# Kernel optimization log

Measured on AMD Instinct MI355X. Metric: run time of the kernel, lower is better.

The kernel has to match this reference:

```python
import jax, jax.numpy as jnp
import numpy as np

P = 200_000   # pedestrians
T = 16        # frames in targets/outputs
F_DIR = 15    # tracklet_length - 5 frames used by direction loss


def _conv_bbox(b):
    # Faithful to the source's in-place convert_bbox, which (due to sequential
    # in-place updates) maps [a,b,c,d] -> [a-c/2, b-d/2, a, b].
    a, bb, c, d = b[..., 0], b[..., 1], b[..., 2], b[..., 3]
    return jnp.stack([a - 0.5 * c, bb - 0.5 * d, a, bb], axis=-1)


def _corner_pts(b):
    # 5 reference points: center, lt(x0,y0), rt(x0,y1), lb(x1,y0), rb(x1,y1)
    x0, y0, x1, y1 = b[..., 0], b[..., 1], b[..., 2], b[..., 3]
    xs = jnp.stack([0.5 * (x0 + x1), x0, x0, x1, x1], axis=-1)
    ys = jnp.stack([0.5 * (y0 + y1), y0, y1, y0, y1], axis=-1)
    return xs, ys


def _unit_dir(fx, fy, tx, ty):
    dy, dx = ty - fy, tx - fx
    n = jnp.sqrt(dy * dy + dx * dx) + 1e-6
    return dy / n, dx / n


def _direction_loss(outputs, targets):
    last = targets[:F_DIR, :, :4]
    pred = last + outputs[:F_DIR]
    true = targets[1:F_DIR + 1, :, :4]
    # Source mutates `targets` in place: frames 1..14 get convert_bbox applied
    # TWICE when reused as `last_abs` (once as prior frame's true_abs). Replicate.
    last_c1 = _conv_bbox(last)
    last_eff = jnp.concatenate([last_c1[:1], _conv_bbox(last_c1[1:])], axis=0)
    pred_c = _conv_bbox(pred)
    true_c = _conv_bbox(true)
    lx, ly = _corner_pts(last_eff)   # [F_DIR, P, 5]
    px, py = _corner_pts(pred_c)
    tx, ty = _corner_pts(true_c)
    pdy, pdx = _unit_dir(lx, ly, px, py)
    tdy, tdx = _unit_dir(lx, ly, tx, ty)
    cosang = jnp.clip(pdy * tdy + pdx * tdx, -1.0, 1.0)
    weight = 0.2
    return weight * jnp.sum(jnp.arccos(cosang)) / (targets.shape[1] * F_DIR)


def setup_inputs() -> dict:
    key = jax.random.key(0)
    k1, k2 = jax.random.split(key)
    outputs = jax.random.normal(k1, (T, P, 4), dtype=jnp.float32) * 0.1
    targets = jax.random.uniform(k2, (T, P, 8), dtype=jnp.float32)
    return {"outputs": outputs, "targets": targets}


def reference(outputs, targets):
    delta = targets[:, :, 4:8]
    d = outputs - delta
    ad = jnp.abs(d)
    sl1 = jnp.where(ad < 1.0, 0.5 * d * d, ad - 0.5)  # smooth_l1, beta=1
    loss_o = jnp.sum(sl1, axis=2) / targets.shape[1]   # [T, P]
    loss_dir = _direction_loss(outputs, targets)
    return 0.99 * loss_o + 0.01 * loss_dir
```

## Files before the change

kernel.cpp:

```cpp
#include <hip/hip_runtime.h>

#define BS 256
#define LD4(ptr) (*reinterpret_cast<const float4*>(ptr))

__device__ __forceinline__ float fast_acos(float x) {
    float ax = fabsf(x);
    float s  = __builtin_amdgcn_sqrtf(fmaxf(0.f, 1.f - ax));
    float p  = fmaf(ax, fmaf(ax, fmaf(ax, -0.0187293f, 0.0742610f), -0.2121144f), 1.5707288f);
    float r  = s * p;
    return (x >= 0.f) ? r : 3.14159265358979f - r;
}

__device__ __forceinline__ float ang(float p2, float t2, float dot) {
    float inv = __builtin_amdgcn_rsqf(p2 * t2);
    float c   = __builtin_amdgcn_fmed3f(dot * inv, -1.f, 1.f);
    return fast_acos(c);
}

__device__ __forceinline__ float dir_item(float4 L, float4 O, float4 Tn, bool first) {
    float pa = L.x + O.x, pb = L.y + O.y;
    float Px0 = pa - 0.5f * (L.z + O.z), Py0 = pb - 0.5f * (L.w + O.w);
    float Px1 = pa, Py1 = pb;
    float Tx0 = Tn.x - 0.5f * Tn.z, Ty0 = Tn.y - 0.5f * Tn.w;
    float Tx1 = Tn.x, Ty1 = Tn.y;
    float Lx1 = L.x - 0.5f * L.z, Ly1 = L.y - 0.5f * L.w;
    float Lx0, Ly0;
    if (first) { Lx0 = Lx1; Ly0 = Ly1; Lx1 = L.x; Ly1 = L.y; }
    else       { Lx0 = 0.5f * (L.x - L.z); Ly0 = 0.5f * (L.y - L.w); }

    float ax0 = Px0 - Lx0, ax1 = Px1 - Lx1, ay0 = Py0 - Ly0, ay1 = Py1 - Ly1;
    float bx0 = Tx0 - Lx0, bx1 = Tx1 - Lx1, by0 = Ty0 - Ly0, by1 = Ty1 - Ly1;
    float acx = 0.5f * (ax0 + ax1), acy = 0.5f * (ay0 + ay1);
    float bcx = 0.5f * (bx0 + bx1), bcy = 0.5f * (by0 + by1);
    float sax0 = ax0 * ax0, sax1 = ax1 * ax1, say0 = ay0 * ay0, say1 = ay1 * ay1;
    float sbx0 = bx0 * bx0, sbx1 = bx1 * bx1, sby0 = by0 * by0, sby1 = by1 * by1;
    float cx0 = ax0 * bx0, cx1 = ax1 * bx1, cy0 = ay0 * by0, cy1 = ay1 * by1;

    float acc;
    acc  = ang(fmaf(acx, acx, acy * acy), fmaf(bcx, bcx, bcy * bcy),
               fmaf(acx, bcx, acy * bcy));
    acc += ang(sax0 + say0, sbx0 + sby0, cx0 + cy0);
    acc += ang(sax0 + say1, sbx0 + sby1, cx0 + cy1);
    acc += ang(sax1 + say0, sbx1 + sby0, cx1 + cy0);
    acc += ang(sax1 + say1, sbx1 + sby1, cx1 + cy1);
    return acc;
}

__device__ __forceinline__ float sl1_4(float4 O, float4 D) {
    float s = 0.f;
    { float d = O.x - D.x, ad = fabsf(d); s += (ad < 1.f) ? 0.5f * d * d : ad - 0.5f; }
    { float d = O.y - D.y, ad = fabsf(d); s += (ad < 1.f) ? 0.5f * d * d : ad - 0.5f; }
    { float d = O.z - D.z, ad = fabsf(d); s += (ad < 1.f) ? 0.5f * d * d : ad - 0.5f; }
    { float d = O.w - D.w, ad = fabsf(d); s += (ad < 1.f) ? 0.5f * d * d : ad - 0.5f; }
    return s;
}

__global__ __launch_bounds__(BS)
void fused_kernel(const float* __restrict__ outputs,
                  const float* __restrict__ targets,
                  float* __restrict__ out,
                  float* __restrict__ partials,
                  int P, float w) {
    __shared__ float smem[BS / 64];
    long long gid = (long long)blockIdx.x * BS + threadIdx.x;
    float acc = 0.f;
    if (gid < 4ll * P) {
        int grp     = (int)(gid / P);
        long long p = gid - (long long)grp * P;
        const long long ts8 = 8ll * P, os4 = 4ll * P;
        const float* tb = targets + ((long long)(grp * 4) * P + p) * 8;
        const float* ob = outputs + ((long long)(grp * 4) * P + p) * 4;
        float*       wb = out + (long long)(grp * 4) * P + p;
        const bool has4 = (grp < 3);

        float4 Tf0 = LD4(tb);
        float4 Tf1 = LD4(tb + ts8);
        float4 Tf2 = LD4(tb + 2 * ts8);
        float4 Tf3 = LD4(tb + 3 * ts8);
        float4 Ts0 = LD4(tb + 4);
        float4 Ts1 = LD4(tb + ts8 + 4);
        float4 Ts2 = LD4(tb + 2 * ts8 + 4);
        float4 Ts3 = LD4(tb + 3 * ts8 + 4);
        float4 O0  = LD4(ob);
        float4 O1  = LD4(ob + os4);
        float4 O2  = LD4(ob + 2 * os4);
        float4 O3  = LD4(ob + 3 * os4);
        float4 Tf4 = has4 ? LD4(tb + 4 * ts8) : make_float4(0.f, 0.f, 0.f, 0.f);

        wb[0]       = sl1_4(O0, Ts0) * w;
        wb[P]       = sl1_4(O1, Ts1) * w;
        wb[2ll * P] = sl1_4(O2, Ts2) * w;
        wb[3ll * P] = sl1_4(O3, Ts3) * w;

        acc  = dir_item(Tf0, O0, Tf1, grp == 0);
        acc += dir_item(Tf1, O1, Tf2, false);
        acc += dir_item(Tf2, O2, Tf3, false);
        if (has4) acc += dir_item(Tf3, O3, Tf4, false);
    }
    #pragma unroll
    for (int off = 32; off > 0; off >>= 1) acc += __shfl_down(acc, off, 64);
    int lane = threadIdx.x & 63, w64 = threadIdx.x >> 6;
    if (lane == 0) smem[w64] = acc;
    __syncthreads();
    if (threadIdx.x == 0) {
        float r = 0.f;
        #pragma unroll
        for (int i = 0; i < BS / 64; ++i) r += smem[i];
        partials[blockIdx.x] = r;
    }
}

__global__ void finalize_kernel(const float* __restrict__ partials, int nb,
                                float* __restrict__ out, long long n4, int P) {
    __shared__ double dsm[BS / 64];
    __shared__ float c_sh;
    double dacc = 0.0;
    for (int i = threadIdx.x; i < nb; i += BS) dacc += (double)partials[i];
    #pragma unroll
    for (int off = 32; off > 0; off >>= 1) dacc += __shfl_down(dacc, off, 64);
    int lane = threadIdx.x & 63, w = threadIdx.x >> 6;
    if (lane == 0) dsm[w] = dacc;
    __syncthreads();
    if (threadIdx.x == 0) {
        double tot = dsm[0] + dsm[1] + dsm[2] + dsm[3];
        c_sh = (float)(0.01 * 0.2 * tot / ((double)P * 15.0));
    }
    __syncthreads();
    float c = c_sh;

    float4* o4 = reinterpret_cast<float4*>(out);
    long long stride = (long long)gridDim.x * blockDim.x;
    for (long long i = (long long)blockIdx.x * blockDim.x + threadIdx.x; i < n4; i += stride) {
        float4 v = o4[i];
        v.x += c; v.y += c; v.z += c; v.w += c;
        o4[i] = v;
    }
}

extern "C" void kernel_launch(void* const* d_in, const int* in_sizes, int n_in,
                              void* d_out, int out_size, void* d_ws, size_t ws_size,
                              hipStream_t stream) {
    const float* outputs = (const float*)d_in[0];
    const float* targets = (const float*)d_in[1];
    float* out = (float*)d_out;
    float* partials = (float*)d_ws;

    const int T = 16;
    int P = in_sizes[0] / (T * 4);

    long long units = 4ll * P;
    int nb1 = (int)((units + BS - 1) / BS);

    fused_kernel<<<nb1, BS, 0, stream>>>(outputs, targets, out, partials,
                                         P, 0.99f / (float)P);

    long long n4 = (long long)out_size / 4;
    int nb2 = (int)((n4 + BS - 1) / BS);
    if (nb2 > 2048) nb2 = 2048;
    finalize_kernel<<<nb2, BS, 0, stream>>>(partials, nb1, out, n4, P);
}
```

Measured before the change: 42.67 us.

## Move smooth-L1 computation into finalize kernel to avoid output read-modify-write

Splits the work so the first kernel computes only the direction-loss partial sums, while the second kernel reduces the partials and computes smooth-L1 per element, writing the final output once. This removes the write-then-reread-and-rewrite of the output buffer. In exchange, outputs and target deltas are re-read in the second kernel, and each kernel reads only half of every target record.

```diff
diff --git a/kernel.cpp b/kernel.cpp
--- a/kernel.cpp
+++ b/kernel.cpp
@@ -46,21 +46,11 @@
     return acc;
 }
 
-__device__ __forceinline__ float sl1_4(float4 O, float4 D) {
-    float s = 0.f;
-    { float d = O.x - D.x, ad = fabsf(d); s += (ad < 1.f) ? 0.5f * d * d : ad - 0.5f; }
-    { float d = O.y - D.y, ad = fabsf(d); s += (ad < 1.f) ? 0.5f * d * d : ad - 0.5f; }
-    { float d = O.z - D.z, ad = fabsf(d); s += (ad < 1.f) ? 0.5f * d * d : ad - 0.5f; }
-    { float d = O.w - D.w, ad = fabsf(d); s += (ad < 1.f) ? 0.5f * d * d : ad - 0.5f; }
-    return s;
-}
-
 __global__ __launch_bounds__(BS)
-void fused_kernel(const float* __restrict__ outputs,
-                  const float* __restrict__ targets,
-                  float* __restrict__ out,
-                  float* __restrict__ partials,
-                  int P, float w) {
+void dir_kernel(const float* __restrict__ outputs,
+                const float* __restrict__ targets,
+                float* __restrict__ partials,
+                int P) {
     __shared__ float smem[BS / 64];
     long long gid = (long long)blockIdx.x * BS + threadIdx.x;
     float acc = 0.f;
@@ -70,27 +60,17 @@
         const long long ts8 = 8ll * P, os4 = 4ll * P;
         const float* tb = targets + ((long long)(grp * 4) * P + p) * 8;
         const float* ob = outputs + ((long long)(grp * 4) * P + p) * 4;
-        float*       wb = out + (long long)(grp * 4) * P + p;
         const bool has4 = (grp < 3);
 
         float4 Tf0 = LD4(tb);
         float4 Tf1 = LD4(tb + ts8);
         float4 Tf2 = LD4(tb + 2 * ts8);
         float4 Tf3 = LD4(tb + 3 * ts8);
-        float4 Ts0 = LD4(tb + 4);
-        float4 Ts1 = LD4(tb + ts8 + 4);
-        float4 Ts2 = LD4(tb + 2 * ts8 + 4);
-        float4 Ts3 = LD4(tb + 3 * ts8 + 4);
         float4 O0  = LD4(ob);
         float4 O1  = LD4(ob + os4);
         float4 O2  = LD4(ob + 2 * os4);
         float4 O3  = LD4(ob + 3 * os4);
         float4 Tf4 = has4 ? LD4(tb + 4 * ts8) : make_float4(0.f, 0.f, 0.f, 0.f);
-
-        wb[0]       = sl1_4(O0, Ts0) * w;
-        wb[P]       = sl1_4(O1, Ts1) * w;
-        wb[2ll * P] = sl1_4(O2, Ts2) * w;
-        wb[3ll * P] = sl1_4(O3, Ts3) * w;
 
         acc  = dir_item(Tf0, O0, Tf1, grp == 0);
         acc += dir_item(Tf1, O1, Tf2, false);
@@ -110,16 +90,20 @@
     }
 }
 
-__global__ void finalize_kernel(const float* __restrict__ partials, int nb,
-                                float* __restrict__ out, long long n4, int P) {
+__global__ __launch_bounds__(BS)
+void out_kernel(const float* __restrict__ outputs,
+                const float* __restrict__ targets,
+                const float* __restrict__ partials, int nb,
+                float* __restrict__ out,
+                long long n, int P, float w) {
     __shared__ double dsm[BS / 64];
     __shared__ float c_sh;
     double dacc = 0.0;
     for (int i = threadIdx.x; i < nb; i += BS) dacc += (double)partials[i];
     #pragma unroll
     for (int off = 32; off > 0; off >>= 1) dacc += __shfl_down(dacc, off, 64);
-    int lane = threadIdx.x & 63, w = threadIdx.x >> 6;
-    if (lane == 0) dsm[w] = dacc;
+    int lane = threadIdx.x & 63, wv = threadIdx.x >> 6;
+    if (lane == 0) dsm[wv] = dacc;
     __syncthreads();
     if (threadIdx.x == 0) {
         double tot = dsm[0] + dsm[1] + dsm[2] + dsm[3];
@@ -128,12 +112,16 @@
     __syncthreads();
     float c = c_sh;
 
-    float4* o4 = reinterpret_cast<float4*>(out);
     long long stride = (long long)gridDim.x * blockDim.x;
-    for (long long i = (long long)blockIdx.x * blockDim.x + threadIdx.x; i < n4; i += stride) {
-        float4 v = o4[i];
-        v.x += c; v.y += c; v.z += c; v.w += c;
-        o4[i] = v;
+    for (long long i = (long long)blockIdx.x * blockDim.x + threadIdx.x; i < n; i += stride) {
+        const float4 O = LD4(outputs + i * 4);
+        const float4 D = LD4(targets + i * 8 + 4);
+        float s = 0.f;
+        { float d = O.x - D.x, ad = fabsf(d); s += (ad < 1.f) ? 0.5f * d * d : ad - 0.5f; }
+        { float d = O.y - D.y, ad = fabsf(d); s += (ad < 1.f) ? 0.5f * d * d : ad - 0.5f; }
+        { float d = O.z - D.z, ad = fabsf(d); s += (ad < 1.f) ? 0.5f * d * d : ad - 0.5f; }
+        { float d = O.w - D.w, ad = fabsf(d); s += (ad < 1.f) ? 0.5f * d * d : ad - 0.5f; }
+        out[i] = fmaf(s, w, c);
     }
 }
 
@@ -150,12 +138,11 @@
 
     long long units = 4ll * P;
     int nb1 = (int)((units + BS - 1) / BS);
+    dir_kernel<<<nb1, BS, 0, stream>>>(outputs, targets, partials, P);
 
-    fused_kernel<<<nb1, BS, 0, stream>>>(outputs, targets, out, partials,
-                                         P, 0.99f / (float)P);
-
-    long long n4 = (long long)out_size / 4;
-    int nb2 = (int)((n4 + BS - 1) / BS);
-    if (nb2 > 2048) nb2 = 2048;
-    finalize_kernel<<<nb2, BS, 0, stream>>>(partials, nb1, out, n4, P);
+    long long n = (long long)out_size;
+    int nb2 = (int)((n + BS - 1) / BS);
+    if (nb2 > 3125) nb2 = 3125;
+    out_kernel<<<nb2, BS, 0, stream>>>(outputs, targets, partials, nb1, out, n, P,
+                                       0.99f / (float)P);
 }
```

New measurement: 60.95 us. 1.43x slower.
